# Kernel tuning notes

Hardware: AMD Instinct MI355X
Metric: run time of the kernel (lower is better)

## Reference

```python
import jax, jax.numpy as jnp
import numpy as np

WINDOW_SIZE = 11
SIGMA = 1.5
C1 = 0.01 ** 2
C2 = 0.03 ** 2


def _gaussian_window(channel, window_size=WINDOW_SIZE, sigma=SIGMA):
    # Faithful to the torch code: the 1D gaussian is NOT normalized.
    x = jnp.arange(window_size, dtype=jnp.float32)
    g = jnp.exp(-((x - window_size // 2) ** 2) / (2.0 * sigma ** 2))
    w2d = jnp.outer(g, g)  # [ws, ws]
    return jnp.broadcast_to(w2d[None, None], (channel, 1, window_size, window_size))


def _dwconv(x, window, window_size, channel):
    # depthwise conv2d with SAME-ish padding = window_size // 2
    pad = window_size // 2
    return jax.lax.conv_general_dilated(
        x, window,
        window_strides=(1, 1),
        padding=[(pad, pad), (pad, pad)],
        dimension_numbers=("NCHW", "OIHW", "NCHW"),
        feature_group_count=channel,
    )


def setup_inputs() -> dict:
    key = jax.random.key(0)
    k1, k2 = jax.random.split(key)
    B, C, H, W = 16, 3, 512, 512
    img1 = jax.random.uniform(k1, (B, C, H, W), dtype=jnp.float32)
    img2 = jax.random.uniform(k2, (B, C, H, W), dtype=jnp.float32)
    return {"img1": img1, "img2": img2}


def reference(img1, img2):
    channel = img1.shape[1]
    window = _gaussian_window(channel).astype(img1.dtype)

    mu1 = _dwconv(img1, window, WINDOW_SIZE, channel)
    mu2 = _dwconv(img2, window, WINDOW_SIZE, channel)
    mu1_sq = mu1 * mu1
    mu2_sq = mu2 * mu2
    mu1_mu2 = mu1 * mu2

    sigma1_sq = _dwconv(img1 * img1, window, WINDOW_SIZE, channel) - mu1_sq
    sigma2_sq = _dwconv(img2 * img2, window, WINDOW_SIZE, channel) - mu2_sq
    sigma12 = _dwconv(img1 * img2, window, WINDOW_SIZE, channel) - mu1_mu2

    ssim_map = ((2.0 * mu1_mu2 + C1) * (2.0 * sigma12 + C2)) / (
        (mu1_sq + mu2_sq + C1) * (sigma1_sq + sigma2_sq + C2)
    )
    # size_average=True -> scalar mean
    return 1.0 - jnp.mean(ssim_map)
```

## Files before the change

### kernel.cpp

```cpp
#include <hip/hip_runtime.h>


typedef float v2f __attribute__((ext_vector_type(2)));

#define IMG   512
#define NIMG  48
#define TW    32
#define TH    32
#define HSTR  46
#define TILES 16
#define NBLOCKS (NIMG * TILES * TILES)

#define G0 0.0038659204f
#define G1 0.0285655010f
#define G2 0.1353352832f
#define G3 0.4111123050f
#define G4 0.8007374029f
#define G5 1.0f

__global__ __launch_bounds__(256, 6) void ssim_tile_kernel(
    const float* __restrict__ img1, const float* __restrict__ img2,
    float* __restrict__ partials)
{
    __shared__ v2f sh2[2][TH][HSTR];
    __shared__ float s_part[4];

    const float gw[11] = {G0,G1,G2,G3,G4,G5,G4,G3,G2,G1,G0};

    const int tid = threadIdx.x;
    const int tx0 = blockIdx.x * TW - 5;
    const int ty0 = blockIdx.y * TH - 5;
    const float* __restrict__ p1 = img1 + (size_t)blockIdx.z * (IMG * IMG);
    const float* __restrict__ p2 = img2 + (size_t)blockIdx.z * (IMG * IMG);

    if (tid < 168) {
        const int c   = tid % 42;
        const int seg = tid / 42;
        const int gc  = tx0 + c;
        const int gr0 = ty0 + seg * 8;

        v2f a0[8], a1[8];
#pragma unroll
        for (int r = 0; r < 8; ++r) { a0[r] = (v2f){0.f, 0.f}; a1[r] = (v2f){0.f, 0.f}; }

        const bool interior = (blockIdx.x >= 1) && (blockIdx.x <= TILES - 2) &&
                              (blockIdx.y >= 1) && (blockIdx.y <= TILES - 2);
        if (interior) {
            const float* q1 = p1 + (size_t)gr0 * IMG + gc;
            const float* q2 = p2 + (size_t)gr0 * IMG + gc;
#pragma unroll
            for (int j = 0; j < 18; ++j) {
                float a = q1[j * IMG], b = q2[j * IMG];
                v2f w0 = (v2f){a + b, a - b};
                v2f w1 = w0 * w0;
#pragma unroll
                for (int r = 0; r < 8; ++r) {
                    int k = j - r;
                    if (k >= 0 && k <= 10) {
                        const v2f wv = {gw[k], gw[k]};
                        a0[r] = __builtin_elementwise_fma(w0, wv, a0[r]);
                        a1[r] = __builtin_elementwise_fma(w1, wv, a1[r]);
                    }
                }
            }
        } else {
            const bool cok = (unsigned)gc < IMG;
#pragma unroll
            for (int j = 0; j < 18; ++j) {
                int gr = gr0 + j;
                bool ok = cok && ((unsigned)gr < IMG);
                float a = 0.f, b = 0.f;
                if (ok) {
                    a = p1[(size_t)gr * IMG + gc];
                    b = p2[(size_t)gr * IMG + gc];
                }
                v2f w0 = (v2f){a + b, a - b};
                v2f w1 = w0 * w0;
#pragma unroll
                for (int r = 0; r < 8; ++r) {
                    int k = j - r;
                    if (k >= 0 && k <= 10) {
                        const v2f wv = {gw[k], gw[k]};
                        a0[r] = __builtin_elementwise_fma(w0, wv, a0[r]);
                        a1[r] = __builtin_elementwise_fma(w1, wv, a1[r]);
                    }
                }
            }
        }
#pragma unroll
        for (int r = 0; r < 8; ++r) {
            sh2[0][seg * 8 + r][c] = a0[r];
            sh2[1][seg * 8 + r][c] = a1[r];
        }
    }
    __syncthreads();

    const int row = tid >> 3;
    const int c0  = (tid & 7) * 4;
    v2f am[4], ax[4];
    {
        v2f hb[14];
        {
            const float4* s0 = (const float4*)&sh2[0][row][c0];
#pragma unroll
            for (int q = 0; q < 7; ++q) ((float4*)hb)[q] = s0[q];
        }
#pragma unroll
        for (int i = 0; i < 4; ++i) {
            v2f s = {0.f, 0.f};
#pragma unroll
            for (int k = 0; k < 11; ++k) {
                const v2f wv = {gw[k], gw[k]};
                s = __builtin_elementwise_fma(wv, hb[i + k], s);
            }
            am[i] = s;
        }
        {
            const float4* s1 = (const float4*)&sh2[1][row][c0];
#pragma unroll
            for (int q = 0; q < 7; ++q) ((float4*)hb)[q] = s1[q];
        }
#pragma unroll
        for (int i = 0; i < 4; ++i) {
            v2f s = {0.f, 0.f};
#pragma unroll
            for (int k = 0; k < 11; ++k) {
                const v2f wv = {gw[k], gw[k]};
                s = __builtin_elementwise_fma(wv, hb[i + k], s);
            }
            ax[i] = s;
        }
    }

    const float C1 = 1.0e-4f, C2 = 9.0e-4f;
    float local = 0.f;
#pragma unroll
    for (int i = 0; i < 4; ++i) {
        v2f mu = am[i];
        v2f mu2 = mu * mu;
        float sum2 = 0.5f  * (mu2[0] + mu2[1]);
        float m12  = 0.25f * (mu2[0] - mu2[1]);
        v2f xx = ax[i];
        float xsum = 0.5f  * (xx[0] + xx[1]);
        float x12  = 0.25f * (xx[0] - xx[1]);
        float sg12  = x12 - m12;
        float sgsum = xsum - sum2;
        float num = (2.f * m12 + C1) * (2.f * sg12 + C2);
        float den = (sum2 + C1) * (sgsum + C2);
        local = fmaf(num, __builtin_amdgcn_rcpf(den), local);
    }

#pragma unroll
    for (int off = 32; off > 0; off >>= 1)
        local += __shfl_down(local, off, 64);
    if ((tid & 63) == 0) s_part[tid >> 6] = local;
    __syncthreads();
    if (tid == 0) {
        int bidx = (blockIdx.z * gridDim.y + blockIdx.y) * gridDim.x + blockIdx.x;
        partials[bidx] = s_part[0] + s_part[1] + s_part[2] + s_part[3];
    }
}

__global__ __launch_bounds__(256) void ssim_final_kernel(
    const float* __restrict__ partials, float* __restrict__ out)
{
    __shared__ double sp[4];
    double acc = 0.0;
    for (int i = threadIdx.x; i < NBLOCKS; i += 256)
        acc += (double)partials[i];
#pragma unroll
    for (int off = 32; off > 0; off >>= 1)
        acc += __shfl_down(acc, off, 64);
    if ((threadIdx.x & 63) == 0) sp[threadIdx.x >> 6] = acc;
    __syncthreads();
    if (threadIdx.x == 0) {
        double total = sp[0] + sp[1] + sp[2] + sp[3];
        out[0] = (float)(1.0 - total / (double)((size_t)NIMG * IMG * IMG));
    }
}

extern "C" void kernel_launch(void* const* d_in, const int* in_sizes, int n_in,
                              void* d_out, int out_size, void* d_ws, size_t ws_size,
                              hipStream_t stream) {
    const float* img1 = (const float*)d_in[0];
    const float* img2 = (const float*)d_in[1];
    float* out = (float*)d_out;
    float* partials = (float*)d_ws;

    dim3 grid(TILES, TILES, NIMG);
    ssim_tile_kernel<<<grid, dim3(256), 0, stream>>>(img1, img2, partials);
    ssim_final_kernel<<<1, dim3(256), 0, stream>>>(partials, out);
}
```

Baseline: 157.0 us.

## Spread vertical pass over 252 threads and batch loads before convolving

The vertical convolution pass now uses 6 row segments (sizes 6,6,5,5,5,5) across 252 threads instead of 4 segments of 8 rows across 168 threads. This raises lane utilisation and cuts per-thread serial FMA work, at the cost of more redundant halo loads (16 or 15 input rows per thread instead of 18 per 8 outputs). All column loads are issued up front into register arrays before computing. The horizontal pass now loads both shared-memory rows together to overlap LDS latency, which costs more registers under the launch bound of 6.

Result: slower. 161.2 us (+2.7%).

```diff
diff --git a/kernel.cpp b/kernel.cpp
--- a/kernel.cpp
+++ b/kernel.cpp
@@ -18,6 +18,35 @@
 #define G4 0.8007374029f
 #define G5 1.0f
 
+template<int SZ>
+__device__ __forceinline__ void vconv_store(
+    const float* __restrict__ ra, const float* __restrict__ rb,
+    const float* __restrict__ gw, v2f (*sh2)[TH][HSTR], int rs, int c)
+{
+    v2f a0[SZ], a1[SZ];
+#pragma unroll
+    for (int r = 0; r < SZ; ++r) { a0[r] = (v2f){0.f, 0.f}; a1[r] = (v2f){0.f, 0.f}; }
+#pragma unroll
+    for (int j = 0; j < SZ + 10; ++j) {
+        v2f w0 = (v2f){ra[j] + rb[j], ra[j] - rb[j]};
+        v2f w1 = w0 * w0;
+#pragma unroll
+        for (int r = 0; r < SZ; ++r) {
+            int k = j - r;
+            if (k >= 0 && k <= 10) {
+                const v2f wv = {gw[k], gw[k]};
+                a0[r] = __builtin_elementwise_fma(w0, wv, a0[r]);
+                a1[r] = __builtin_elementwise_fma(w1, wv, a1[r]);
+            }
+        }
+    }
+#pragma unroll
+    for (int r = 0; r < SZ; ++r) {
+        sh2[0][rs + r][c] = a0[r];
+        sh2[1][rs + r][c] = a1[r];
+    }
+}
+
 __global__ __launch_bounds__(256, 6) void ssim_tile_kernel(
     const float* __restrict__ img1, const float* __restrict__ img2,
     float* __restrict__ partials)
@@ -33,65 +62,39 @@
     const float* __restrict__ p1 = img1 + (size_t)blockIdx.z * (IMG * IMG);
     const float* __restrict__ p2 = img2 + (size_t)blockIdx.z * (IMG * IMG);
 
-    if (tid < 168) {
+    if (tid < 252) {
         const int c   = tid % 42;
         const int seg = tid / 42;
+        const int sz  = (seg < 2) ? 6 : 5;
+        const int rs  = (seg < 2) ? seg * 6 : 12 + (seg - 2) * 5;
+        const int nin = sz + 10;
         const int gc  = tx0 + c;
-        const int gr0 = ty0 + seg * 8;
+        const int gr0 = ty0 + rs;
 
-        v2f a0[8], a1[8];
-#pragma unroll
-        for (int r = 0; r < 8; ++r) { a0[r] = (v2f){0.f, 0.f}; a1[r] = (v2f){0.f, 0.f}; }
-
+        float ra[16], rb[16];
         const bool interior = (blockIdx.x >= 1) && (blockIdx.x <= TILES - 2) &&
                               (blockIdx.y >= 1) && (blockIdx.y <= TILES - 2);
         if (interior) {
             const float* q1 = p1 + (size_t)gr0 * IMG + gc;
             const float* q2 = p2 + (size_t)gr0 * IMG + gc;
 #pragma unroll
-            for (int j = 0; j < 18; ++j) {
-                float a = q1[j * IMG], b = q2[j * IMG];
-                v2f w0 = (v2f){a + b, a - b};
-                v2f w1 = w0 * w0;
-#pragma unroll
-                for (int r = 0; r < 8; ++r) {
-                    int k = j - r;
-                    if (k >= 0 && k <= 10) {
-                        const v2f wv = {gw[k], gw[k]};
-                        a0[r] = __builtin_elementwise_fma(w0, wv, a0[r]);
-                        a1[r] = __builtin_elementwise_fma(w1, wv, a1[r]);
-                    }
-                }
+            for (int j = 0; j < 16; ++j) {
+                if (j < nin) { ra[j] = q1[j * IMG]; rb[j] = q2[j * IMG]; }
             }
         } else {
             const bool cok = (unsigned)gc < IMG;
 #pragma unroll
-            for (int j = 0; j < 18; ++j) {
-                int gr = gr0 + j;
-                bool ok = cok && ((unsigned)gr < IMG);
-                float a = 0.f, b = 0.f;
-                if (ok) {
-                    a = p1[(size_t)gr * IMG + gc];
-                    b = p2[(size_t)gr * IMG + gc];
-                }
-                v2f w0 = (v2f){a + b, a - b};
-                v2f w1 = w0 * w0;
-#pragma unroll
-                for (int r = 0; r < 8; ++r) {
-                    int k = j - r;
-                    if (k >= 0 && k <= 10) {
-                        const v2f wv = {gw[k], gw[k]};
-                        a0[r] = __builtin_elementwise_fma(w0, wv, a0[r]);
-                        a1[r] = __builtin_elementwise_fma(w1, wv, a1[r]);
-                    }
+            for (int j = 0; j < 16; ++j) {
+                if (j < nin) {
+                    int gr = gr0 + j;
+                    bool ok = cok && ((unsigned)gr < IMG);
+                    ra[j] = ok ? p1[(size_t)gr * IMG + gc] : 0.f;
+                    rb[j] = ok ? p2[(size_t)gr * IMG + gc] : 0.f;
                 }
             }
         }
-#pragma unroll
-        for (int r = 0; r < 8; ++r) {
-            sh2[0][seg * 8 + r][c] = a0[r];
-            sh2[1][seg * 8 + r][c] = a1[r];
-        }
+        if (sz == 6) vconv_store<6>(ra, rb, gw, sh2, rs, c);
+        else         vconv_store<5>(ra, rb, gw, sh2, rs, c);
     }
     __syncthreads();
 
@@ -99,11 +102,14 @@
     const int c0  = (tid & 7) * 4;
     v2f am[4], ax[4];
     {
-        v2f hb[14];
+        v2f hb0[14], hb1[14];
         {
             const float4* s0 = (const float4*)&sh2[0][row][c0];
+            const float4* s1 = (const float4*)&sh2[1][row][c0];
 #pragma unroll
-            for (int q = 0; q < 7; ++q) ((float4*)hb)[q] = s0[q];
+            for (int q = 0; q < 7; ++q) ((float4*)hb0)[q] = s0[q];
+#pragma unroll
+            for (int q = 0; q < 7; ++q) ((float4*)hb1)[q] = s1[q];
         }
 #pragma unroll
         for (int i = 0; i < 4; ++i) {
@@ -111,14 +117,9 @@
 #pragma unroll
             for (int k = 0; k < 11; ++k) {
                 const v2f wv = {gw[k], gw[k]};
-                s = __builtin_elementwise_fma(wv, hb[i + k], s);
+                s = __builtin_elementwise_fma(wv, hb0[i + k], s);
             }
             am[i] = s;
-        }
-        {
-            const float4* s1 = (const float4*)&sh2[1][row][c0];
-#pragma unroll
-            for (int q = 0; q < 7; ++q) ((float4*)hb)[q] = s1[q];
         }
 #pragma unroll
         for (int i = 0; i < 4; ++i) {
@@ -126,7 +127,7 @@
 #pragma unroll
             for (int k = 0; k < 11; ++k) {
                 const v2f wv = {gw[k], gw[k]};
-                s = __builtin_elementwise_fma(wv, hb[i + k], s);
+                s = __builtin_elementwise_fma(wv, hb1[i + k], s);
             }
             ax[i] = s;
         }
```
